# Kernel optimization log

Hardware: AMD Instinct MI355X
Metric: run time of the kernel (lower is better)

Reference implementation:

```python
import jax, jax.numpy as jnp
import numpy as np

B, T, C, D = 64, 4096, 51, 64
MASK_PROB = 0.3
LN_EPS = 1e-5


def setup_inputs() -> dict:
    key = jax.random.key(0)
    k0, k1, k2, k3, k4 = jax.random.split(key, 5)
    x = jax.random.normal(k0, (B, T, C), dtype=jnp.float32)
    # xavier_uniform_ then *= 0.5 (as in reset_parameters)
    bound = float(np.sqrt(6.0 / (C + D)))
    W = jax.random.uniform(k1, (C, D), jnp.float32, -bound, bound) * 0.5
    Wm = jax.random.uniform(k2, (C, D), jnp.float32, -bound, bound) * 0.5
    gamma = jnp.ones((D,), jnp.float32)
    beta = jnp.zeros((D,), jnp.float32)
    time_mask = jax.random.bernoulli(k3, MASK_PROB, (B, T))
    sensor_mask = jax.random.bernoulli(k4, MASK_PROB, (B, C))
    return {"x": x, "W": W, "Wm": Wm, "gamma": gamma, "beta": beta,
            "time_mask": time_mask, "sensor_mask": sensor_mask}


def reference(x, W, Wm, gamma, beta, time_mask, sensor_mask):
    # mask[b,t,c] = time_mask[b,t] OR sensor_mask[b,c]
    mask = (time_mask[:, :, None] | sensor_mask[:, None, :]).astype(x.dtype)  # [B,T,C]
    # Fused masked reductions (math-equivalent to the broadcast [B,T,C,D] path)
    xu = jnp.einsum('btc,cd->btd', x * (1.0 - mask), W)   # [B,T,D]
    xm = jnp.einsum('btc,cd->btd', mask, Wm)              # [B,T,D]
    out = xu + xm
    # LayerNorm over last dim
    mu = jnp.mean(out, axis=-1, keepdims=True)
    var = jnp.mean((out - mu) ** 2, axis=-1, keepdims=True)
    out = (out - mu) * jax.lax.rsqrt(var + LN_EPS) * gamma + beta
    return out
```

## Files before the change

kernel.cpp:

```cpp
#include <hip/hip_runtime.h>

#define BB 64
#define TT 4096
#define CC 51
#define DD 64
#define LN_EPS 1e-5f

typedef __attribute__((ext_vector_type(8))) short short8;
typedef __attribute__((ext_vector_type(4))) float f32x4;

union FragU { int i[4]; short8 s; };

#define DPP_QP_1032   0xB1
#define DPP_QP_2301   0x4E
#define DPP_ROW_HMIRR 0x141
#define DPP_ROW_MIRR  0x140

__device__ __forceinline__ float dpp_add(float v, int tag) {
  int t;
  switch (tag) {
    case 0: t = __builtin_amdgcn_update_dpp(0, __float_as_int(v), DPP_QP_1032,   0xF, 0xF, true); break;
    case 1: t = __builtin_amdgcn_update_dpp(0, __float_as_int(v), DPP_QP_2301,   0xF, 0xF, true); break;
    case 2: t = __builtin_amdgcn_update_dpp(0, __float_as_int(v), DPP_ROW_HMIRR, 0xF, 0xF, true); break;
    default: t = __builtin_amdgcn_update_dpp(0, __float_as_int(v), DPP_ROW_MIRR, 0xF, 0xF, true); break;
  }
  return v + __int_as_float(t);
}
__device__ __forceinline__ float allsum16(float v) {
  v = dpp_add(v, 0); v = dpp_add(v, 1); v = dpp_add(v, 2); v = dpp_add(v, 3);
  return v;
}
__device__ __forceinline__ float allsum64(float v) {
  v = allsum16(v);
  v += __shfl_xor(v, 16, 64);
  v += __shfl_xor(v, 32, 64);
  return v;
}

__device__ __forceinline__ int pack_hl(float x) {
  const unsigned u = __float_as_uint(x);
  const unsigned h = u >> 16;
  const float hf = __uint_as_float(u & 0xFFFF0000u);
  const unsigned l = __float_as_uint(x - hf) >> 16;
  return (int)(h | (l << 16));
}

__global__ void ipmask_setup3(const float* __restrict__ Wm,
                              const float* __restrict__ gamma,
                              const float* __restrict__ beta,
                              const int* __restrict__ smask,
                              float* __restrict__ ws) {
  __shared__ float red[8][64];
  const int t = threadIdx.x, L = t & 63, w = t >> 6;
  const int b = blockIdx.x;
  const int c0 = w * 13, c1 = (c0 + 13 < CC) ? c0 + 13 : CC;
  float bs = 0.0f, f = 0.0f;
  for (int c = c0; c < c1; ++c) {
    const float wmv = Wm[c * DD + L];
    const float sf = (float)smask[b * CC + c];
    bs = fmaf(sf, wmv, bs);
    f += wmv;
  }
  red[w * 2][L] = bs;
  red[w * 2 + 1][L] = f;
  __syncthreads();
  if (w == 0) {
    bs = (red[0][L] + red[2][L]) + (red[4][L] + red[6][L]);
    f  = (red[1][L] + red[3][L]) + (red[5][L] + red[7][L]);
    ws[b * 128 + L] = bs;
    const float s1 = allsum64(f);
    const float s2 = allsum64(f * f);
    const float mu = s1 * (1.0f / 64.0f);
    const float vr = fmaf(-mu, mu, s2 * (1.0f / 64.0f));
    const float rs = rsqrtf(vr + LN_EPS);
    ws[b * 128 + 64 + L] = fmaf((f - mu) * rs, gamma[L], beta[L]);
  }
}

__global__ __launch_bounds__(256, 2)
void ipmask_mfma3(const float* __restrict__ x, const float* __restrict__ W,
                  const float* __restrict__ gamma, const float* __restrict__ beta,
                  const int* __restrict__ tmask, const int* __restrict__ smask,
                  const float* __restrict__ ws, float* __restrict__ out) {
  const int t = threadIdx.x, L = t & 63;
  const int q = L >> 4, m16 = L & 15;
  const int gw = (blockIdx.x << 2) + (t >> 6);
  const int b = gw >> 6;
  const int rowBase = (b << 12) + ((gw & 63) << 6);

  const int* smB = smask + b * CC;

  float xf[4][4][4];
#pragma unroll
  for (int mt = 0; mt < 4; ++mt) {
    const float* xr = x + (size_t)(rowBase + mt * 16 + m16) * CC;
#pragma unroll
    for (int ks = 0; ks < 4; ++ks) {
#pragma unroll
      for (int j = 0; j < 4; ++j) {
        const int c = ks * 16 + q * 4 + j;
        xf[mt][ks][j] = (c < CC) ? xr[c] : 0.0f;
      }
    }
  }
  const int tmv = tmask[rowBase + L];

  f32x4 acc[4][4];
#pragma unroll
  for (int nt = 0; nt < 4; ++nt) {
    const float bias_nt = ws[b * 128 + nt * 16 + m16];
#pragma unroll
    for (int mt = 0; mt < 4; ++mt) {
      acc[mt][nt][0] = bias_nt; acc[mt][nt][1] = bias_nt;
      acc[mt][nt][2] = bias_nt; acc[mt][nt][3] = bias_nt;
    }
  }

#pragma unroll
  for (int ks = 0; ks < 4; ++ks) {
    FragU bmu[4], bcu[4];
#pragma unroll
    for (int j = 0; j < 4; ++j) {
      const int c = ks * 16 + q * 4 + j;
      const int smv = (c < CC) ? smB[c] : 1;
#pragma unroll
      for (int nt = 0; nt < 4; ++nt) {
        const int n = nt * 16 + m16;
        float we = 0.0f;
        if (c < CC) we = W[c * DD + n];
        if (smv) we = 0.0f;
        const unsigned u = __float_as_uint(we);
        const unsigned h = u >> 16;
        const float hf = __uint_as_float(u & 0xFFFF0000u);
        const unsigned l = __float_as_uint(we - hf) >> 16;
        bmu[nt].i[j] = (int)(h | (h << 16));
        bcu[nt].i[j] = (int)l;
      }
    }
#pragma unroll
    for (int mt = 0; mt < 4; ++mt) {
      FragU au;
#pragma unroll
      for (int j = 0; j < 4; ++j) au.i[j] = pack_hl(xf[mt][ks][j]);
#pragma unroll
      for (int nt = 0; nt < 4; ++nt) {
        acc[mt][nt] = __builtin_amdgcn_mfma_f32_16x16x32_bf16(au.s, bmu[nt].s, acc[mt][nt], 0, 0, 0);
        acc[mt][nt] = __builtin_amdgcn_mfma_f32_16x16x32_bf16(au.s, bcu[nt].s, acc[mt][nt], 0, 0, 0);
      }
    }
  }

  float g_[4], b_[4], cons_[4];
#pragma unroll
  for (int nt = 0; nt < 4; ++nt) {
    g_[nt] = gamma[nt * 16 + m16];
    b_[nt] = beta[nt * 16 + m16];
    cons_[nt] = ws[b * 128 + 64 + nt * 16 + m16];
  }
#pragma unroll
  for (int mt = 0; mt < 4; ++mt) {
#pragma unroll
    for (int rg = 0; rg < 4; ++rg) {
      float su = 0.0f, sq = 0.0f;
#pragma unroll
      for (int nt = 0; nt < 4; ++nt) {
        const float v = acc[mt][nt][rg];
        su += v;
        sq = fmaf(v, v, sq);
      }
      su = allsum16(su);
      sq = allsum16(sq);
      const float mu = su * (1.0f / 64.0f);
      const float vr = fmaf(-mu, mu, sq * (1.0f / 64.0f));
      const float rs = rsqrtf(vr + LN_EPS);
      const int rloc = mt * 16 + q * 4 + rg;
      const int tm = __shfl(tmv, rloc, 64);
      const size_t obase = (size_t)(rowBase + rloc) * DD;
#pragma unroll
      for (int nt = 0; nt < 4; ++nt) {
        float val = fmaf((acc[mt][nt][rg] - mu) * rs, g_[nt], b_[nt]);
        if (tm) val = cons_[nt];
        __builtin_nontemporal_store(val, &out[obase + nt * 16 + m16]);
      }
    }
  }
}

extern "C" void kernel_launch(void* const* d_in, const int* in_sizes, int n_in,
                              void* d_out, int out_size, void* d_ws, size_t ws_size,
                              hipStream_t stream) {
  const float* x     = (const float*)d_in[0];
  const float* W     = (const float*)d_in[1];
  const float* Wm    = (const float*)d_in[2];
  const float* gamma = (const float*)d_in[3];
  const float* beta  = (const float*)d_in[4];
  const int*   tmask = (const int*)d_in[5];
  const int*   smask = (const int*)d_in[6];
  float* out = (float*)d_out;
  float* ws  = (float*)d_ws;

  ipmask_setup3<<<dim3(BB), dim3(256), 0, stream>>>(Wm, gamma, beta, smask, ws);
  ipmask_mfma3<<<dim3(1024), dim3(256), 0, stream>>>(
      x, W, gamma, beta, tmask, smask, ws, out);
}
```

Measured before the change: 128.7 us.

## Precompute packed bf16 hi/lo W fragments in setup kernel; mask x instead of W

The extra setup block now splits W into bf16 high/low pairs once and stores them as an MFMA-ready fragment table in workspace. The main kernel loads these fragments with vector loads and no longer does per-block scalar loads of W and the split arithmetic. The sensor mask moves from W onto x, and rows that are time-masked skip their x loads entirely. This trades ALU and scalar-load work for table reads from workspace and some divergence on the x loads.

```diff
diff --git a/kernel.cpp b/kernel.cpp
--- a/kernel.cpp
+++ b/kernel.cpp
@@ -8,8 +8,9 @@
 
 typedef __attribute__((ext_vector_type(8))) short short8;
 typedef __attribute__((ext_vector_type(4))) float f32x4;
-
-union FragU { int i[4]; short8 s; };
+typedef __attribute__((ext_vector_type(4))) int i32x4;
+
+union FragU { int i[4]; i32x4 v; short8 s; };
 
 #define DPP_QP_1032   0xB1
 #define DPP_QP_2301   0x4E
@@ -45,13 +46,33 @@
   return (int)(h | (l << 16));
 }
 
-__global__ void ipmask_setup3(const float* __restrict__ Wm,
+__global__ void ipmask_setup4(const float* __restrict__ W,
+                              const float* __restrict__ Wm,
                               const float* __restrict__ gamma,
                               const float* __restrict__ beta,
                               const int* __restrict__ smask,
                               float* __restrict__ ws) {
+  const int t = threadIdx.x;
+  if (blockIdx.x >= BB) {
+    int* tabMU = (int*)(ws + 2 * BB * DD);
+    int* tabCU = tabMU + 4096;
+#pragma unroll
+    for (int e = 0; e < 16; ++e) {
+      const int idx = t * 16 + e;
+      const int j = idx & 3, qq = (idx >> 2) & 3, n = (idx >> 4) & 63, ks = idx >> 10;
+      const int c = ks * 16 + qq * 4 + j;
+      const float w = (c < CC) ? W[c * DD + n] : 0.0f;
+      const unsigned u = __float_as_uint(w);
+      const unsigned h = u >> 16;
+      const float hf = __uint_as_float(u & 0xFFFF0000u);
+      const unsigned l = __float_as_uint(w - hf) >> 16;
+      tabMU[idx] = (int)(h | (h << 16));
+      tabCU[idx] = (int)l;
+    }
+    return;
+  }
   __shared__ float red[8][64];
-  const int t = threadIdx.x, L = t & 63, w = t >> 6;
+  const int L = t & 63, w = t >> 6;
   const int b = blockIdx.x;
   const int c0 = w * 13, c1 = (c0 + 13 < CC) ? c0 + 13 : CC;
   float bs = 0.0f, f = 0.0f;
@@ -78,7 +99,7 @@
 }
 
 __global__ __launch_bounds__(256, 2)
-void ipmask_mfma3(const float* __restrict__ x, const float* __restrict__ W,
+void ipmask_mfma4(const float* __restrict__ x,
                   const float* __restrict__ gamma, const float* __restrict__ beta,
                   const int* __restrict__ tmask, const int* __restrict__ smask,
                   const float* __restrict__ ws, float* __restrict__ out) {
@@ -89,21 +110,41 @@
   const int rowBase = (b << 12) + ((gw & 63) << 6);
 
   const int* smB = smask + b * CC;
+  const int* tabMU = (const int*)(ws + 2 * BB * DD);
+  const int* tabCU = tabMU + 4096;
+
+  const int tmv = tmask[rowBase + L];
+
+  float msk[4][4];
+#pragma unroll
+  for (int ks = 0; ks < 4; ++ks)
+#pragma unroll
+    for (int j = 0; j < 4; ++j) {
+      const int c = ks * 16 + q * 4 + j;
+      const int sv = (c < CC) ? smB[c] : 1;
+      msk[ks][j] = sv ? 0.0f : 1.0f;
+    }
 
   float xf[4][4][4];
 #pragma unroll
   for (int mt = 0; mt < 4; ++mt) {
+    const int tm_r = __shfl(tmv, mt * 16 + m16, 64);
     const float* xr = x + (size_t)(rowBase + mt * 16 + m16) * CC;
-#pragma unroll
-    for (int ks = 0; ks < 4; ++ks) {
-#pragma unroll
-      for (int j = 0; j < 4; ++j) {
-        const int c = ks * 16 + q * 4 + j;
-        xf[mt][ks][j] = (c < CC) ? xr[c] : 0.0f;
-      }
-    }
-  }
-  const int tmv = tmask[rowBase + L];
+    if (!tm_r) {
+#pragma unroll
+      for (int ks = 0; ks < 4; ++ks)
+#pragma unroll
+        for (int j = 0; j < 4; ++j) {
+          const int c = ks * 16 + q * 4 + j;
+          xf[mt][ks][j] = (c < CC) ? xr[c] * msk[ks][j] : 0.0f;
+        }
+    } else {
+#pragma unroll
+      for (int ks = 0; ks < 4; ++ks)
+#pragma unroll
+        for (int j = 0; j < 4; ++j) xf[mt][ks][j] = 0.0f;
+    }
+  }
 
   f32x4 acc[4][4];
 #pragma unroll
@@ -120,22 +161,10 @@
   for (int ks = 0; ks < 4; ++ks) {
     FragU bmu[4], bcu[4];
 #pragma unroll
-    for (int j = 0; j < 4; ++j) {
-      const int c = ks * 16 + q * 4 + j;
-      const int smv = (c < CC) ? smB[c] : 1;
-#pragma unroll
-      for (int nt = 0; nt < 4; ++nt) {
-        const int n = nt * 16 + m16;
-        float we = 0.0f;
-        if (c < CC) we = W[c * DD + n];
-        if (smv) we = 0.0f;
-        const unsigned u = __float_as_uint(we);
-        const unsigned h = u >> 16;
-        const float hf = __uint_as_float(u & 0xFFFF0000u);
-        const unsigned l = __float_as_uint(we - hf) >> 16;
-        bmu[nt].i[j] = (int)(h | (h << 16));
-        bcu[nt].i[j] = (int)l;
-      }
+    for (int nt = 0; nt < 4; ++nt) {
+      const int base = ks * 1024 + (nt * 16 + m16) * 16 + q * 4;
+      bmu[nt].v = *(const i32x4*)&tabMU[base];
+      bcu[nt].v = *(const i32x4*)&tabCU[base];
     }
 #pragma unroll
     for (int mt = 0; mt < 4; ++mt) {
@@ -199,7 +228,7 @@
   float* out = (float*)d_out;
   float* ws  = (float*)d_ws;
 
-  ipmask_setup3<<<dim3(BB), dim3(256), 0, stream>>>(Wm, gamma, beta, smask, ws);
-  ipmask_mfma3<<<dim3(1024), dim3(256), 0, stream>>>(
-      x, W, gamma, beta, tmask, smask, ws, out);
-}
+  ipmask_setup4<<<dim3(BB + 1), dim3(256), 0, stream>>>(W, Wm, gamma, beta, smask, ws);
+  ipmask_mfma4<<<dim3(1024), dim3(256), 0, stream>>>(
+      x, gamma, beta, tmask, smask, ws, out);
+}
```

Result: slower. 137.9 us (+7.2%).
